# Optimization experiments

Hardware: AMD Instinct MI355X
Metric: run time of the kernel (lower is better)

Reference implementation:

```python
import jax, jax.numpy as jnp
import numpy as np

B, S, D = 4, 4096, 1024
E, I = 8, 2048
CAPACITY = 2
K = max(1, int(S / E * CAPACITY))  # tokens per expert per batch element


def setup_inputs() -> dict:
    key = jax.random.key(0)
    k1, k2, k3, k4, k5 = jax.random.split(key, 5)
    x = jax.random.normal(k1, (B, S, D), dtype=jnp.float32)
    gate_w = jax.random.normal(k2, (D, E), dtype=jnp.float32) * 0.006
    Wg = jax.random.normal(k3, (E, D, I), dtype=jnp.float32) * 0.02
    Wu = jax.random.normal(k4, (E, D, I), dtype=jnp.float32) * 0.02
    Wd = jax.random.normal(k5, (E, I, D), dtype=jnp.float32) * 0.02
    return {"x": x, "gate_w": gate_w, "Wg": Wg, "Wu": Wu, "Wd": Wd}


def reference(x, gate_w, Wg, Wu, Wd):
    # Router: softmax over experts per token, then per-expert top-k tokens.
    logits = jnp.einsum('bsd,de->bse', x, gate_w)          # [B,S,E]
    affinity = jax.nn.softmax(logits, axis=-1)
    affinity_T = jnp.transpose(affinity, (0, 2, 1))        # [B,E,S]
    gating, index = jax.lax.top_k(affinity_T, K)           # [B,E,K]

    # Gather selected tokens for all experts at once: [B,E,K,D]
    b_idx = jnp.arange(x.shape[0])[:, None, None]
    x_sel = x[b_idx, index]

    # Per-expert SwiGLU MLP (grouped GEMMs over the expert axis).
    g = jnp.einsum('bekd,edi->beki', x_sel, Wg)
    u = jnp.einsum('bekd,edi->beki', x_sel, Wu)
    h = jax.nn.silu(g) * u
    out = jnp.einsum('beki,eid->bekd', h, Wd)              # [B,E,K,D]

    # Weighted scatter-add combine back to token positions.
    contrib = out * gating[..., None]
    x_out = jnp.zeros_like(x).at[b_idx, index].add(contrib)
    return x_out
```

## Files before the change

kernel.cpp:

```cpp
#include <hip/hip_runtime.h>

#define B_ 4
#define S_ 4096
#define D_ 1024
#define E_ 8
#define I_ 2048
#define K_ 1024

typedef __attribute__((ext_vector_type(8))) short short8;
typedef __attribute__((ext_vector_type(4))) float f32x4;

__device__ __forceinline__ short f2bf(float f) {
  union { float f; unsigned u; } v; v.f = f;
  unsigned r = v.u + 0x7FFFu + ((v.u >> 16) & 1u);
  return (short)(r >> 16);
}

__device__ __forceinline__ void gload16(const void* g, void* l) {
  __builtin_amdgcn_global_load_lds((const __attribute__((address_space(1))) unsigned int*)g,
                                   (__attribute__((address_space(3))) unsigned int*)l, 16, 0, 0);
}

__device__ __forceinline__ short8 rdswz(const short* ls, int row, int cb) {
  int byte = (row << 7) + (cb ^ ((row & 7) << 4));
  return *reinterpret_cast<const short8*>(reinterpret_cast<const char*>(ls) + byte);
}

__global__ __launch_bounds__(256) void router_kernel(const float* __restrict__ x,
                                                     const float* __restrict__ gw,
                                                     double* __restrict__ affD) {
  int wave = threadIdx.x >> 6, lane = threadIdx.x & 63;
  int tok = blockIdx.x * 4 + wave;
  int b = tok >> 12, s = tok & (S_ - 1);
  const float* xr = x + (size_t)tok * D_;
  double acc[E_];
#pragma unroll
  for (int e = 0; e < E_; ++e) acc[e] = 0.0;
#pragma unroll 4
  for (int r = 0; r < 16; ++r) {
    int d = r * 64 + lane;
    float xv = xr[d];
    const float4* g4 = reinterpret_cast<const float4*>(gw + (size_t)d * E_);
    float4 g0 = g4[0], g1 = g4[1];
    acc[0] += (double)xv * g0.x; acc[1] += (double)xv * g0.y;
    acc[2] += (double)xv * g0.z; acc[3] += (double)xv * g0.w;
    acc[4] += (double)xv * g1.x; acc[5] += (double)xv * g1.y;
    acc[6] += (double)xv * g1.z; acc[7] += (double)xv * g1.w;
  }
#pragma unroll
  for (int off = 32; off > 0; off >>= 1) {
#pragma unroll
    for (int e = 0; e < E_; ++e) acc[e] += __shfl_xor(acc[e], off, 64);
  }
  double m = acc[0];
#pragma unroll
  for (int e = 1; e < E_; ++e) m = acc[e] > m ? acc[e] : m;
  double den = 0.0, ex[E_];
#pragma unroll
  for (int e = 0; e < E_; ++e) { ex[e] = exp(acc[e] - m); den += ex[e]; }
  if (lane < E_)
    affD[((size_t)b * E_ + lane) * S_ + s] = ex[lane] / den;
}

__global__ __launch_bounds__(1024) void topk_kernel(const double* __restrict__ affD,
                                                    int* __restrict__ idxArr,
                                                    float* __restrict__ gateArr) {
  __shared__ unsigned long long keys[S_];
  __shared__ int sidx[S_];
  int be = blockIdx.x, tid = threadIdx.x;
  const double* a = affD + (size_t)be * S_;
  for (int t = tid; t < S_; t += 1024) {
    keys[t] = (unsigned long long)__double_as_longlong(a[t]);
    sidx[t] = t;
  }
  __syncthreads();
  for (int k = 2; k <= S_; k <<= 1) {
    for (int j = k >> 1; j > 0; j >>= 1) {
      for (int t = tid; t < S_; t += 1024) {
        int x2 = t ^ j;
        if (x2 > t) {
          unsigned long long ka = keys[t], kb = keys[x2];
          int ia = sidx[t], ib = sidx[x2];
          bool agt = (ka > kb) || (ka == kb && ia < ib);
          bool up = ((t & k) == 0);
          if (up == agt) {
            keys[t] = kb; keys[x2] = ka;
            sidx[t] = ib; sidx[x2] = ia;
          }
        }
      }
      __syncthreads();
    }
  }
  for (int t = tid; t < K_; t += 1024) {
    int p = S_ - 1 - t;
    gateArr[(size_t)be * K_ + t] = (float)__longlong_as_double((long long)keys[p]);
    idxArr[(size_t)be * K_ + t] = sidx[p];
  }
}

__global__ __launch_bounds__(256) void transpose_cvt_kernel(const float* __restrict__ in,
                                                            unsigned short* __restrict__ out,
                                                            int M, int N) {
  __shared__ float t[64][65];
  int e = blockIdx.y;
  int ntn = N >> 6;
  int tm = (blockIdx.x / ntn) << 6;
  int tn = (blockIdx.x % ntn) << 6;
  const float* src = in + (size_t)e * M * N;
  unsigned short* dst = out + (size_t)e * M * N;
  int tid = threadIdx.x;
#pragma unroll
  for (int it = 0; it < 4; ++it) {
    int f = it * 256 + tid;
    int r = f >> 4, c4 = (f & 15) << 2;
    float4 v = *reinterpret_cast<const float4*>(&src[(size_t)(tm + r) * N + tn + c4]);
    t[c4][r] = v.x; t[c4 + 1][r] = v.y; t[c4 + 2][r] = v.z; t[c4 + 3][r] = v.w;
  }
  __syncthreads();
#pragma unroll
  for (int it = 0; it < 4; ++it) {
    int f = it * 256 + tid;
    int rr = f >> 4, c4 = (f & 15) << 2;
    short4 o;
    o.x = f2bf(t[rr][c4]); o.y = f2bf(t[rr][c4 + 1]);
    o.z = f2bf(t[rr][c4 + 2]); o.w = f2bf(t[rr][c4 + 3]);
    *reinterpret_cast<short4*>(&dst[(size_t)(tn + rr) * M + tm + c4]) = o;
  }
}

__global__ __launch_bounds__(256) void gather_cvt_kernel(const float* __restrict__ x,
                                                         const int* __restrict__ idxArr,
                                                         unsigned short* __restrict__ Xsel) {
  int row = blockIdx.x * 4 + (threadIdx.x >> 6);
  int lane = threadIdx.x & 63;
  int b = row >> 13;
  int tok = idxArr[row];
  const float* src = x + ((size_t)b * S_ + tok) * D_;
  unsigned short* dst = Xsel + (size_t)row * D_;
#pragma unroll
  for (int it = 0; it < 4; ++it) {
    int d = it * 256 + lane * 4;
    float4 v = *reinterpret_cast<const float4*>(src + d);
    short4 o;
    o.x = f2bf(v.x); o.y = f2bf(v.y); o.z = f2bf(v.z); o.w = f2bf(v.w);
    *reinterpret_cast<short4*>(dst + d) = o;
  }
}

__global__ __launch_bounds__(256, 2) void mlp1_kernel(
    const unsigned short* __restrict__ Xsel, const unsigned short* __restrict__ WgT,
    const unsigned short* __restrict__ WuT, unsigned short* __restrict__ H,
    int Ic, int i0) {
  const int Nt = Ic >> 7;
  int nwg = gridDim.x;
  int bid = (blockIdx.x & 7) * (nwg >> 3) + (blockIdx.x >> 3);
  int nt = bid % Nt; bid /= Nt;
  int mt = bid & 7; bid >>= 3;
  int be = bid;
  int e = be & 7;

  __shared__ short lsA[128 * 64];
  __shared__ short lsBg[128 * 64];
  __shared__ short lsBu[128 * 64];

  int tid = threadIdx.x, w = tid >> 6, lane = tid & 63;
  int wm = w >> 1, wn = w & 1;
  int lr = lane & 15, lg = lane >> 4;

  const char* pa = (const char*)(Xsel + ((size_t)be * K_ + mt * 128) * D_);
  const char* pg = (const char*)(WgT + (size_t)e * I_ * D_ + (size_t)(i0 + nt * 128) * D_);
  const char* pu = (const char*)(WuT + (size_t)e * I_ * D_ + (size_t)(i0 + nt * 128) * D_);

  int srow = lane >> 3;
  int scol = ((lane & 7) ^ srow) << 4;

  f32x4 accg[4][4], accu[4][4];
#pragma unroll
  for (int i = 0; i < 4; ++i)
#pragma unroll
    for (int j = 0; j < 4; ++j) {
      accg[i][j] = (f32x4){0.f, 0.f, 0.f, 0.f};
      accu[i][j] = (f32x4){0.f, 0.f, 0.f, 0.f};
    }

  for (int k0 = 0; k0 < D_; k0 += 64) {
#pragma unroll
    for (int c = 0; c < 4; ++c) {
      int chunk = c * 4 + w;
      int row = chunk * 8 + srow;
      size_t go = (size_t)row * (D_ * 2) + (size_t)k0 * 2 + scol;
      gload16(pa + go, (char*)lsA + chunk * 1024);
      gload16(pg + go, (char*)lsBg + chunk * 1024);
      gload16(pu + go, (char*)lsBu + chunk * 1024);
    }
    __syncthreads();
#pragma unroll
    for (int fk = 0; fk < 2; ++fk) {
      int cb = fk * 64 + lg * 16;
      short8 af[4], bgf[4], buf[4];
#pragma unroll
      for (int fm = 0; fm < 4; ++fm)
        af[fm] = rdswz(lsA, wm * 64 + fm * 16 + lr, cb);
#pragma unroll
      for (int fn = 0; fn < 4; ++fn) {
        bgf[fn] = rdswz(lsBg, wn * 64 + fn * 16 + lr, cb);
        buf[fn] = rdswz(lsBu, wn * 64 + fn * 16 + lr, cb);
      }
#pragma unroll
      for (int fm = 0; fm < 4; ++fm)
#pragma unroll
        for (int fn = 0; fn < 4; ++fn) {
          accg[fm][fn] = __builtin_amdgcn_mfma_f32_16x16x32_bf16(af[fm], bgf[fn], accg[fm][fn], 0, 0, 0);
          accu[fm][fn] = __builtin_amdgcn_mfma_f32_16x16x32_bf16(af[fm], buf[fn], accu[fm][fn], 0, 0, 0);
        }
    }
    __syncthreads();
  }
  unsigned short* Hbe = H + (size_t)be * K_ * Ic;
#pragma unroll
  for (int fm = 0; fm < 4; ++fm)
#pragma unroll
    for (int fn = 0; fn < 4; ++fn) {
#pragma unroll
      for (int j = 0; j < 4; ++j) {
        float g = accg[fm][fn][j], u = accu[fm][fn][j];
        float h = g / (1.f + __expf(-g)) * u;
        int row = wm * 64 + fm * 16 + lg * 4 + j;
        int col = wn * 64 + fn * 16 + lr;
        Hbe[(size_t)(mt * 128 + row) * Ic + nt * 128 + col] = (unsigned short)f2bf(h);
      }
    }
}

__global__ __launch_bounds__(256, 2) void mlp2_kernel(
    const unsigned short* __restrict__ H, const unsigned short* __restrict__ WdT,
    const int* __restrict__ idxArr, const float* __restrict__ gateArr,
    float* __restrict__ out, int Ic, int i0) {
  int nwg = gridDim.x;
  int bid = (blockIdx.x & 7) * (nwg >> 3) + (blockIdx.x >> 3);
  int nt = bid & 7; bid >>= 3;
  int mt = bid & 7; bid >>= 3;
  int be = bid;
  int b = be >> 3, e = be & 7;

  __shared__ short lsA[128 * 64];
  __shared__ short lsB[128 * 64];
  __shared__ int sTok[128];
  __shared__ float sGate[128];

  int tid = threadIdx.x;
  if (tid < 128) {
    sTok[tid] = idxArr[(size_t)be * K_ + mt * 128 + tid];
    sGate[tid] = gateArr[(size_t)be * K_ + mt * 128 + tid];
  }

  const char* pa = (const char*)(H + ((size_t)be * K_ + mt * 128) * Ic);
  const char* pb = (const char*)(WdT + (size_t)e * D_ * I_ + (size_t)(nt * 128) * I_ + i0);

  int w = tid >> 6, lane = tid & 63;
  int wm = w >> 1, wn = w & 1;
  int lr = lane & 15, lg = lane >> 4;

  int srow = lane >> 3;
  int scol = ((lane & 7) ^ srow) << 4;

  f32x4 acc[4][4];
#pragma unroll
  for (int i = 0; i < 4; ++i)
#pragma unroll
    for (int j = 0; j < 4; ++j) acc[i][j] = (f32x4){0.f, 0.f, 0.f, 0.f};

  for (int k0 = 0; k0 < Ic; k0 += 64) {
#pragma unroll
    for (int c = 0; c < 4; ++c) {
      int chunk = c * 4 + w;
      int row = chunk * 8 + srow;
      gload16(pa + (size_t)row * (Ic * 2) + (size_t)k0 * 2 + scol, (char*)lsA + chunk * 1024);
      gload16(pb + (size_t)row * (I_ * 2) + (size_t)k0 * 2 + scol, (char*)lsB + chunk * 1024);
    }
    __syncthreads();
#pragma unroll
    for (int fk = 0; fk < 2; ++fk) {
      int cb = fk * 64 + lg * 16;
      short8 af[4], bf[4];
#pragma unroll
      for (int fm = 0; fm < 4; ++fm)
        af[fm] = rdswz(lsA, wm * 64 + fm * 16 + lr, cb);
#pragma unroll
      for (int fn = 0; fn < 4; ++fn)
        bf[fn] = rdswz(lsB, wn * 64 + fn * 16 + lr, cb);
#pragma unroll
      for (int fm = 0; fm < 4; ++fm)
#pragma unroll
        for (int fn = 0; fn < 4; ++fn)
          acc[fm][fn] = __builtin_amdgcn_mfma_f32_16x16x32_bf16(af[fm], bf[fn], acc[fm][fn], 0, 0, 0);
    }
    __syncthreads();
  }
#pragma unroll
  for (int fm = 0; fm < 4; ++fm)
#pragma unroll
    for (int fn = 0; fn < 4; ++fn) {
#pragma unroll
      for (int j = 0; j < 4; ++j) {
        int row = wm * 64 + fm * 16 + lg * 4 + j;
        int col = nt * 128 + wn * 64 + fn * 16 + lr;
        float v = acc[fm][fn][j] * sGate[row];
        atomicAdd(&out[((size_t)b * S_ + sTok[row]) * D_ + col], v);
      }
    }
}

extern "C" void kernel_launch(void* const* d_in, const int* in_sizes, int n_in,
                              void* d_out, int out_size, void* d_ws, size_t ws_size,
                              hipStream_t stream) {
  const float* x  = (const float*)d_in[0];
  const float* gw = (const float*)d_in[1];
  const float* Wg = (const float*)d_in[2];
  const float* Wu = (const float*)d_in[3];
  const float* Wd = (const float*)d_in[4];
  float* out = (float*)d_out;
  char* ws = (char*)d_ws;

  size_t off = 0;
  double* affD = (double*)(ws + off); off += (size_t)B_ * E_ * S_ * sizeof(double);
  int* idxArr = (int*)(ws + off);     off += (size_t)B_ * E_ * K_ * sizeof(int);
  float* gateArr = (float*)(ws + off); off += (size_t)B_ * E_ * K_ * sizeof(float);
  off = (off + 255) & ~(size_t)255;
  unsigned short* WgT = (unsigned short*)(ws + off); off += (size_t)E_ * D_ * I_ * 2;
  unsigned short* WuT = (unsigned short*)(ws + off); off += (size_t)E_ * D_ * I_ * 2;
  unsigned short* WdT = (unsigned short*)(ws + off); off += (size_t)E_ * D_ * I_ * 2;
  unsigned short* Xsel = (unsigned short*)(ws + off); off += (size_t)B_ * E_ * K_ * D_ * 2;
  off = (off + 255) & ~(size_t)255;
  unsigned short* H = (unsigned short*)(ws + off);
  size_t rem = (ws_size > off) ? (ws_size - off) : 0;

  int Ic = 128;
  for (int c = I_; c >= 128; c >>= 1) {
    if ((size_t)B_ * E_ * K_ * (size_t)c * 2 <= rem) { Ic = c; break; }
  }

  hipMemsetAsync(d_out, 0, (size_t)out_size * sizeof(float), stream);
  router_kernel<<<B_ * S_ / 4, 256, 0, stream>>>(x, gw, affD);
  topk_kernel<<<B_ * E_, 1024, 0, stream>>>(affD, idxArr, gateArr);
  transpose_cvt_kernel<<<dim3((D_ / 64) * (I_ / 64), E_), 256, 0, stream>>>(Wg, WgT, D_, I_);
  transpose_cvt_kernel<<<dim3((D_ / 64) * (I_ / 64), E_), 256, 0, stream>>>(Wu, WuT, D_, I_);
  transpose_cvt_kernel<<<dim3((I_ / 64) * (D_ / 64), E_), 256, 0, stream>>>(Wd, WdT, I_, D_);
  gather_cvt_kernel<<<B_ * E_ * K_ / 4, 256, 0, stream>>>(x, idxArr, Xsel);
  for (int i0 = 0; i0 < I_; i0 += Ic) {
    mlp1_kernel<<<B_ * E_ * 8 * (Ic / 128), 256, 0, stream>>>(Xsel, WgT, WuT, H, Ic, i0);
    mlp2_kernel<<<B_ * E_ * 8 * 8, 256, 0, stream>>>(H, WdT, idxArr, gateArr, out, Ic, i0);
  }
}
```

Baseline: 801.2 us.

## Use radix select for top-k, fuse gather into MLP1, chunk tokens instead of I

The bitonic sort of 4096 keys per (batch, expert) is replaced by an 8-pass radix select with a shared histogram, with the token index packed into the low bits of the key for tie-breaking. The separate gather kernel is removed: x is converted to bf16 once, and mlp1 loads the selected rows directly through per-row token indices. The MLP loop now splits the K tokens into two halves over the full I dimension instead of chunking I, and the occupancy hints change. This cuts sort cost and an extra gathered copy, but alters top-k ordering and loses the low 12 bits of the key. It also assumes the workspace can hold H for half the tokens.

```diff
diff --git a/kernel.cpp b/kernel.cpp
--- a/kernel.cpp
+++ b/kernel.cpp
@@ -62,40 +62,62 @@
     affD[((size_t)b * E_ + lane) * S_ + s] = ex[lane] / den;
 }
 
-__global__ __launch_bounds__(1024) void topk_kernel(const double* __restrict__ affD,
-                                                    int* __restrict__ idxArr,
-                                                    float* __restrict__ gateArr) {
-  __shared__ unsigned long long keys[S_];
-  __shared__ int sidx[S_];
+__global__ __launch_bounds__(1024) void topk_select_kernel(const double* __restrict__ affD,
+                                                           int* __restrict__ idxArr,
+                                                           float* __restrict__ gateArr) {
+  __shared__ unsigned hist[256];
+  __shared__ unsigned s_digit;
+  __shared__ int s_rem;
+  __shared__ unsigned s_cnt;
   int be = blockIdx.x, tid = threadIdx.x;
   const double* a = affD + (size_t)be * S_;
-  for (int t = tid; t < S_; t += 1024) {
-    keys[t] = (unsigned long long)__double_as_longlong(a[t]);
-    sidx[t] = t;
-  }
+  unsigned long long key[4];
+  bool active[4];
+#pragma unroll
+  for (int c = 0; c < 4; ++c) {
+    int i = tid + c * 1024;
+    unsigned long long kb = (unsigned long long)__double_as_longlong(a[i]);
+    key[c] = (kb & ~0xFFFULL) | (unsigned long long)(4095 - i);
+    active[c] = true;
+  }
+  int remk = K_;
+  unsigned long long prefix = 0;
+  for (int pass = 0; pass < 8; ++pass) {
+    int shift = 56 - pass * 8;
+    if (tid < 256) hist[tid] = 0;
+    __syncthreads();
+#pragma unroll
+    for (int c = 0; c < 4; ++c)
+      if (active[c]) atomicAdd(&hist[(unsigned)((key[c] >> shift) & 0xFF)], 1u);
+    __syncthreads();
+    if (tid == 0) {
+      unsigned cum = 0; int d = 255;
+      for (; d > 0; --d) {
+        unsigned h = hist[d];
+        if (cum + h >= (unsigned)remk) break;
+        cum += h;
+      }
+      s_digit = (unsigned)d;
+      s_rem = remk - (int)cum;
+    }
+    __syncthreads();
+    unsigned dg = s_digit; remk = s_rem;
+    prefix |= ((unsigned long long)dg) << shift;
+#pragma unroll
+    for (int c = 0; c < 4; ++c)
+      active[c] = active[c] && (((key[c] >> shift) & 0xFF) == dg);
+    __syncthreads();
+  }
+  if (tid == 0) s_cnt = 0;
   __syncthreads();
-  for (int k = 2; k <= S_; k <<= 1) {
-    for (int j = k >> 1; j > 0; j >>= 1) {
-      for (int t = tid; t < S_; t += 1024) {
-        int x2 = t ^ j;
-        if (x2 > t) {
-          unsigned long long ka = keys[t], kb = keys[x2];
-          int ia = sidx[t], ib = sidx[x2];
-          bool agt = (ka > kb) || (ka == kb && ia < ib);
-          bool up = ((t & k) == 0);
-          if (up == agt) {
-            keys[t] = kb; keys[x2] = ka;
-            sidx[t] = ib; sidx[x2] = ia;
-          }
-        }
-      }
-      __syncthreads();
-    }
-  }
-  for (int t = tid; t < K_; t += 1024) {
-    int p = S_ - 1 - t;
-    gateArr[(size_t)be * K_ + t] = (float)__longlong_as_double((long long)keys[p]);
-    idxArr[(size_t)be * K_ + t] = sidx[p];
+#pragma unroll
+  for (int c = 0; c < 4; ++c) {
+    if (key[c] >= prefix) {
+      unsigned slot = atomicAdd(&s_cnt, 1u);
+      int i = 4095 - (int)(key[c] & 0xFFF);
+      idxArr[(size_t)be * K_ + slot] = i;
+      gateArr[(size_t)be * K_ + slot] = (float)a[i];
+    }
   }
 }
 
@@ -129,36 +151,27 @@
   }
 }
 
-__global__ __launch_bounds__(256) void gather_cvt_kernel(const float* __restrict__ x,
-                                                         const int* __restrict__ idxArr,
-                                                         unsigned short* __restrict__ Xsel) {
-  int row = blockIdx.x * 4 + (threadIdx.x >> 6);
-  int lane = threadIdx.x & 63;
-  int b = row >> 13;
-  int tok = idxArr[row];
-  const float* src = x + ((size_t)b * S_ + tok) * D_;
-  unsigned short* dst = Xsel + (size_t)row * D_;
-#pragma unroll
-  for (int it = 0; it < 4; ++it) {
-    int d = it * 256 + lane * 4;
-    float4 v = *reinterpret_cast<const float4*>(src + d);
-    short4 o;
-    o.x = f2bf(v.x); o.y = f2bf(v.y); o.z = f2bf(v.z); o.w = f2bf(v.w);
-    *reinterpret_cast<short4*>(dst + d) = o;
-  }
-}
-
-__global__ __launch_bounds__(256, 2) void mlp1_kernel(
-    const unsigned short* __restrict__ Xsel, const unsigned short* __restrict__ WgT,
-    const unsigned short* __restrict__ WuT, unsigned short* __restrict__ H,
-    int Ic, int i0) {
-  const int Nt = Ic >> 7;
+__global__ __launch_bounds__(256) void cvt_bf16_kernel(const float* __restrict__ x,
+                                                       unsigned short* __restrict__ Xbf) {
+  size_t i = ((size_t)blockIdx.x * 256 + threadIdx.x) * 8;
+  float4 a = *reinterpret_cast<const float4*>(x + i);
+  float4 b = *reinterpret_cast<const float4*>(x + i + 4);
+  short8 t;
+  t[0] = f2bf(a.x); t[1] = f2bf(a.y); t[2] = f2bf(a.z); t[3] = f2bf(a.w);
+  t[4] = f2bf(b.x); t[5] = f2bf(b.y); t[6] = f2bf(b.z); t[7] = f2bf(b.w);
+  *reinterpret_cast<short8*>(Xbf + i) = t;
+}
+
+__global__ __launch_bounds__(256, 3) void mlp1_kernel(
+    const unsigned short* __restrict__ Xbf, const unsigned short* __restrict__ WgT,
+    const unsigned short* __restrict__ WuT, const int* __restrict__ idxArr,
+    unsigned short* __restrict__ H, int kc) {
   int nwg = gridDim.x;
   int bid = (blockIdx.x & 7) * (nwg >> 3) + (blockIdx.x >> 3);
-  int nt = bid % Nt; bid /= Nt;
-  int mt = bid & 7; bid >>= 3;
+  int nt = bid & 15; bid >>= 4;
+  int mt = bid & 3; bid >>= 2;
   int be = bid;
-  int e = be & 7;
+  int b = be >> 3, e = be & 7;
 
   __shared__ short lsA[128 * 64];
   __shared__ short lsBg[128 * 64];
@@ -168,12 +181,17 @@
   int wm = w >> 1, wn = w & 1;
   int lr = lane & 15, lg = lane >> 4;
 
-  const char* pa = (const char*)(Xsel + ((size_t)be * K_ + mt * 128) * D_);
-  const char* pg = (const char*)(WgT + (size_t)e * I_ * D_ + (size_t)(i0 + nt * 128) * D_);
-  const char* pu = (const char*)(WuT + (size_t)e * I_ * D_ + (size_t)(i0 + nt * 128) * D_);
-
   int srow = lane >> 3;
   int scol = ((lane & 7) ^ srow) << 4;
+
+  int tokR[4];
+#pragma unroll
+  for (int c = 0; c < 4; ++c)
+    tokR[c] = idxArr[(size_t)be * K_ + kc * 512 + mt * 128 + (c * 4 + w) * 8 + srow];
+
+  const char* xb = (const char*)(Xbf + (size_t)b * S_ * D_);
+  const char* pg = (const char*)(WgT + (size_t)e * I_ * D_ + (size_t)(nt * 128) * D_);
+  const char* pu = (const char*)(WuT + (size_t)e * I_ * D_ + (size_t)(nt * 128) * D_);
 
   f32x4 accg[4][4], accu[4][4];
 #pragma unroll
@@ -189,10 +207,11 @@
     for (int c = 0; c < 4; ++c) {
       int chunk = c * 4 + w;
       int row = chunk * 8 + srow;
-      size_t go = (size_t)row * (D_ * 2) + (size_t)k0 * 2 + scol;
-      gload16(pa + go, (char*)lsA + chunk * 1024);
-      gload16(pg + go, (char*)lsBg + chunk * 1024);
-      gload16(pu + go, (char*)lsBu + chunk * 1024);
+      size_t gw_ = (size_t)row * (D_ * 2) + (size_t)k0 * 2 + scol;
+      size_t ga = ((size_t)tokR[c] * D_ + k0) * 2 + scol;
+      gload16(xb + ga, (char*)lsA + chunk * 1024);
+      gload16(pg + gw_, (char*)lsBg + chunk * 1024);
+      gload16(pu + gw_, (char*)lsBu + chunk * 1024);
     }
     __syncthreads();
 #pragma unroll
@@ -217,7 +236,7 @@
     }
     __syncthreads();
   }
-  unsigned short* Hbe = H + (size_t)be * K_ * Ic;
+  unsigned short* Hbe = H + (size_t)be * 512 * I_;
 #pragma unroll
   for (int fm = 0; fm < 4; ++fm)
 #pragma unroll
@@ -228,19 +247,19 @@
         float h = g / (1.f + __expf(-g)) * u;
         int row = wm * 64 + fm * 16 + lg * 4 + j;
         int col = wn * 64 + fn * 16 + lr;
-        Hbe[(size_t)(mt * 128 + row) * Ic + nt * 128 + col] = (unsigned short)f2bf(h);
+        Hbe[(size_t)(mt * 128 + row) * I_ + nt * 128 + col] = (unsigned short)f2bf(h);
       }
     }
 }
 
-__global__ __launch_bounds__(256, 2) void mlp2_kernel(
+__global__ __launch_bounds__(256, 4) void mlp2_kernel(
     const unsigned short* __restrict__ H, const unsigned short* __restrict__ WdT,
     const int* __restrict__ idxArr, const float* __restrict__ gateArr,
-    float* __restrict__ out, int Ic, int i0) {
+    float* __restrict__ out, int kc) {
   int nwg = gridDim.x;
   int bid = (blockIdx.x & 7) * (nwg >> 3) + (blockIdx.x >> 3);
   int nt = bid & 7; bid >>= 3;
-  int mt = bid & 7; bid >>= 3;
+  int mt = bid & 3; bid >>= 2;
   int be = bid;
   int b = be >> 3, e = be & 7;
 
@@ -251,12 +270,13 @@
 
   int tid = threadIdx.x;
   if (tid < 128) {
-    sTok[tid] = idxArr[(size_t)be * K_ + mt * 128 + tid];
-    sGate[tid] = gateArr[(size_t)be * K_ + mt * 128 + tid];
-  }
-
-  const char* pa = (const char*)(H + ((size_t)be * K_ + mt * 128) * Ic);
-  const char* pb = (const char*)(WdT + (size_t)e * D_ * I_ + (size_t)(nt * 128) * I_ + i0);
+    size_t gbase = (size_t)be * K_ + kc * 512 + mt * 128 + tid;
+    sTok[tid] = idxArr[gbase];
+    sGate[tid] = gateArr[gbase];
+  }
+
+  const char* pa = (const char*)(H + ((size_t)be * 512 + mt * 128) * I_);
+  const char* pb = (const char*)(WdT + (size_t)e * D_ * I_ + (size_t)(nt * 128) * I_);
 
   int w = tid >> 6, lane = tid & 63;
   int wm = w >> 1, wn = w & 1;
@@ -271,13 +291,14 @@
 #pragma unroll
     for (int j = 0; j < 4; ++j) acc[i][j] = (f32x4){0.f, 0.f, 0.f, 0.f};
 
-  for (int k0 = 0; k0 < Ic; k0 += 64) {
+  for (int k0 = 0; k0 < I_; k0 += 64) {
 #pragma unroll
     for (int c = 0; c < 4; ++c) {
       int chunk = c * 4 + w;
       int row = chunk * 8 + srow;
-      gload16(pa + (size_t)row * (Ic * 2) + (size_t)k0 * 2 + scol, (char*)lsA + chunk * 1024);
-      gload16(pb + (size_t)row * (I_ * 2) + (size_t)k0 * 2 + scol, (char*)lsB + chunk * 1024);
+      size_t go = (size_t)row * (I_ * 2) + (size_t)k0 * 2 + scol;
+      gload16(pa + go, (char*)lsA + chunk * 1024);
+      gload16(pb + go, (char*)lsB + chunk * 1024);
     }
     __syncthreads();
 #pragma unroll
@@ -331,25 +352,19 @@
   unsigned short* WgT = (unsigned short*)(ws + off); off += (size_t)E_ * D_ * I_ * 2;
   unsigned short* WuT = (unsigned short*)(ws + off); off += (size_t)E_ * D_ * I_ * 2;
   unsigned short* WdT = (unsigned short*)(ws + off); off += (size_t)E_ * D_ * I_ * 2;
-  unsigned short* Xsel = (unsigned short*)(ws + off); off += (size_t)B_ * E_ * K_ * D_ * 2;
+  unsigned short* Xbf = (unsigned short*)(ws + off); off += (size_t)B_ * S_ * D_ * 2;
   off = (off + 255) & ~(size_t)255;
   unsigned short* H = (unsigned short*)(ws + off);
-  size_t rem = (ws_size > off) ? (ws_size - off) : 0;
-
-  int Ic = 128;
-  for (int c = I_; c >= 128; c >>= 1) {
-    if ((size_t)B_ * E_ * K_ * (size_t)c * 2 <= rem) { Ic = c; break; }
-  }
 
   hipMemsetAsync(d_out, 0, (size_t)out_size * sizeof(float), stream);
   router_kernel<<<B_ * S_ / 4, 256, 0, stream>>>(x, gw, affD);
-  topk_kernel<<<B_ * E_, 1024, 0, stream>>>(affD, idxArr, gateArr);
+  topk_select_kernel<<<B_ * E_, 1024, 0, stream>>>(affD, idxArr, gateArr);
   transpose_cvt_kernel<<<dim3((D_ / 64) * (I_ / 64), E_), 256, 0, stream>>>(Wg, WgT, D_, I_);
   transpose_cvt_kernel<<<dim3((D_ / 64) * (I_ / 64), E_), 256, 0, stream>>>(Wu, WuT, D_, I_);
   transpose_cvt_kernel<<<dim3((I_ / 64) * (D_ / 64), E_), 256, 0, stream>>>(Wd, WdT, I_, D_);
-  gather_cvt_kernel<<<B_ * E_ * K_ / 4, 256, 0, stream>>>(x, idxArr, Xsel);
-  for (int i0 = 0; i0 < I_; i0 += Ic) {
-    mlp1_kernel<<<B_ * E_ * 8 * (Ic / 128), 256, 0, stream>>>(Xsel, WgT, WuT, H, Ic, i0);
-    mlp2_kernel<<<B_ * E_ * 8 * 8, 256, 0, stream>>>(H, WdT, idxArr, gateArr, out, Ic, i0);
-  }
-}
+  cvt_bf16_kernel<<<(B_ * S_ * D_) / 2048, 256, 0, stream>>>(x, Xbf);
+  for (int kc = 0; kc < 2; ++kc) {
+    mlp1_kernel<<<B_ * E_ * 4 * 16, 256, 0, stream>>>(Xbf, WgT, WuT, idxArr, H, kc);
+    mlp2_kernel<<<B_ * E_ * 4 * 8, 256, 0, stream>>>(H, WdT, idxArr, gateArr, out, kc);
+  }
+}
```

Measured after the change: 1.040 ms. 1.3x slower.
